# Performance work log

Measured on AMD Instinct MI355X. Metric: run time of the kernel, lower is better.

The kernel has to match this reference:

```python
import jax, jax.numpy as jnp
import numpy as np
from jax import lax


def setup_inputs() -> dict:
    key = jax.random.key(0)
    k1, k2, k3, k4 = jax.random.split(key, 4)
    B, K, Hp, Wp = 512, 64, 5, 5
    num_classes = 10
    x = jax.random.uniform(k1, (B, 1, 20, 20), dtype=jnp.float32)
    patterns = jax.random.uniform(k2, (K, 1, Hp, Wp), dtype=jnp.float32)
    w2 = jax.random.normal(k3, (1, K), dtype=jnp.float32) * 0.1
    b2 = jnp.zeros((1,), dtype=jnp.float32)
    wf = jax.random.normal(k4, (num_classes, 400), dtype=jnp.float32) * 0.05
    bf = jnp.zeros((num_classes,), dtype=jnp.float32)
    return {"x": x, "patterns": patterns, "w2": w2, "b2": b2, "wf": wf, "bf": bf}


def _geneo1(patterns, x):
    # patterns: (K,1,Hp,Wp), x: (B,1,H,W). Same-padded sliding L1 similarity.
    K, _, Hp, Wp = patterns.shape
    P = Hp * Wp
    xp = jnp.pad(x, ((0, 0), (0, 0), (Hp // 2, Hp // 2), (Wp // 2, Wp // 2)))
    # (B, P, H_out, W_out); C=1 so feature order is row-major over (Hp,Wp),
    # matching torch's unfold(2,Hp,1).unfold(3,Wp,1).reshape(-1).
    patches = lax.conv_general_dilated_patches(xp, (Hp, Wp), (1, 1), "VALID")
    pat = patterns.reshape(K, P)
    # (B,K,H_out,W_out): mean_|p| |pattern - patch|
    diff = jnp.abs(pat[None, :, :, None, None] - patches[:, None, :, :, :]).mean(axis=2)
    return 1.0 - diff


def _channel_wise_max(t):
    B, K, H, W = t.shape
    flat = t.reshape(B, K, H * W)
    idx = jnp.argmax(flat, axis=2)                      # (B,K)
    mask = jax.nn.one_hot(idx, H * W, dtype=flat.dtype) # (B,K,HW)
    return (flat * mask).reshape(B, K, H, W)


def reference(x, patterns, w2, b2, wf, bf):
    Fk = _geneo1(patterns, x)            # (B,K,20,20)
    cwm = _channel_wise_max(Fk)          # (B,K,20,20)
    # GENEO2: Linear(K,1) over channel dim (applied on (B,H,W,K))
    t = jnp.einsum("bkhw,ok->bhwo", cwm, w2) + b2   # (B,20,20,1)
    t = jax.nn.sigmoid(t)
    out = t.reshape(t.shape[0], -1) @ wf.T + bf      # (B,num_classes)
    return jax.nn.sigmoid(out)
```

## Files before the change

### kernel.cpp

```cpp
#include <hip/hip_runtime.h>
#include <math.h>

#define NB 512
#define NK 64
#define HW 400
#define NC 10

__device__ __forceinline__ unsigned sad16(unsigned a, unsigned b, unsigned c) {
#if __has_builtin(__builtin_amdgcn_sad_u16)
    return __builtin_amdgcn_sad_u16(a, b, c);
#else
    unsigned d;
    asm("v_sad_u16 %0, %1, %2, %3" : "=v"(d) : "v"(a), "v"(b), "v"(c));
    return d;
#endif
}

__global__ __launch_bounds__(1024, 1) void geneo_mlp_kernel(
    const float* __restrict__ x,
    const float* __restrict__ patterns,
    const float* __restrict__ w2,
    const float* __restrict__ b2,
    const float* __restrict__ wf,
    const float* __restrict__ bf,
    float* __restrict__ out)
{
    __shared__ __align__(16) unsigned xq4[4][576];
    __shared__ __align__(16) unsigned pqd4[4][552];
    __shared__ __align__(16) float pat_lds[NK * 25];
    __shared__ unsigned redbest[16][NK];
    __shared__ float2 pixcv[NK];
    __shared__ float colsum[NC];
    __shared__ float redout[NC];

    const int tid  = threadIdx.x;
    const int b    = blockIdx.x;
    const int lane = tid & 63;
    const int wave = tid >> 6;

    if (tid < 576) {
        const int h = tid / 24, w = tid - h * 24;
        float v = 0.f;
        if (h >= 2 && h < 22 && w >= 2 && w < 22)
            v = x[b * HW + (h - 2) * 20 + (w - 2)];
        xq4[0][tid] = (unsigned)(v * 65535.f + 0.5f);
    } else if (tid < 976) {
        const int i = tid - 576;
        reinterpret_cast<float4*>(pat_lds)[i] =
            reinterpret_cast<const float4*>(patterns)[i];
    }
    __syncthreads();

    for (int i = tid; i < 3 * 576; i += 1024) {
        const int j = i / 576 + 1;
        const int w = i - (j - 1) * 576;
        int src = w + j; if (src > 575) src = 575;
        xq4[j][w] = xq4[0][src];
    }
    __syncthreads();

    for (int i = tid; i < 4 * 552; i += 1024) {
        const int j = i / 552;
        const int w = i - j * 552;
        pqd4[j][w] = xq4[j][w] | (xq4[j][w + 24] << 16);
    }

    unsigned vp01[5], vp23[5], p4v[5];
    #pragma unroll
    for (int c = 0; c < 5; ++c) {
        const unsigned q0 = (unsigned)(pat_lds[lane * 25 +  0 + c] * 65535.f + 0.5f);
        const unsigned q1 = (unsigned)(pat_lds[lane * 25 +  5 + c] * 65535.f + 0.5f);
        const unsigned q2 = (unsigned)(pat_lds[lane * 25 + 10 + c] * 65535.f + 0.5f);
        const unsigned q3 = (unsigned)(pat_lds[lane * 25 + 15 + c] * 65535.f + 0.5f);
        const unsigned q4 = (unsigned)(pat_lds[lane * 25 + 20 + c] * 65535.f + 0.5f);
        vp01[c] = q0 | (q1 << 16);
        vp23[c] = q2 | (q3 << 16);
        p4v[c]  = q4;
    }
    __syncthreads();

    const int tr   = wave >> 2;
    const int tc   = wave & 3;
    const int base = 4 * tc;
    unsigned best  = 0xFFFFFFFFu;

    #pragma unroll 1
    for (int r = 0; r < 5; ++r) {
        const int h = tr * 5 + r;
        const unsigned* r01 = &pqd4[tc][h * 24 + base];
        const unsigned* r23 = &pqd4[tc][(h + 2) * 24 + base];
        const unsigned* r4  = &xq4[tc][(h + 4) * 24 + base];
        uint4 A0 = *reinterpret_cast<const uint4*>(r01);
        uint4 A1 = *reinterpret_cast<const uint4*>(r01 + 4);
        unsigned A8 = r01[8];
        uint4 B0 = *reinterpret_cast<const uint4*>(r23);
        uint4 B1 = *reinterpret_cast<const uint4*>(r23 + 4);
        unsigned B8 = r23[8];
        uint4 C0 = *reinterpret_cast<const uint4*>(r4);
        uint4 C1 = *reinterpret_cast<const uint4*>(r4 + 4);
        unsigned C8 = r4[8];
        const unsigned W01[9] = {A0.x, A0.y, A0.z, A0.w, A1.x, A1.y, A1.z, A1.w, A8};
        const unsigned W23[9] = {B0.x, B0.y, B0.z, B0.w, B1.x, B1.y, B1.z, B1.w, B8};
        const unsigned W4 [9] = {C0.x, C0.y, C0.z, C0.w, C1.x, C1.y, C1.z, C1.w, C8};
        #pragma unroll
        for (int px = 0; px < 5; ++px) {
            unsigned s = 0;
            #pragma unroll
            for (int dx = 0; dx < 5; ++dx) {
                s = sad16(W01[px + dx], vp01[dx], s);
                s = sad16(W23[px + dx], vp23[dx], s);
                s = sad16(W4 [px + dx], p4v [dx], s);
            }
            const unsigned pk = (s << 9) | (unsigned)(h * 20 + tc * 5 + px);
            best = min(best, pk);
        }
    }
    redbest[wave][lane] = best;
    __syncthreads();

    if (wave < NC) {
        float sc = 0.f;
        for (int p = lane; p < HW; p += 64) sc += wf[wave * HW + p];
        #pragma unroll
        for (int off = 32; off >= 1; off >>= 1) sc += __shfl_down(sc, off);
        if (lane == 0) colsum[wave] = sc;
    }
    if (wave == 15) {
        unsigned b0 = redbest[0][lane];
        #pragma unroll
        for (int w = 1; w < 16; ++w) b0 = min(b0, redbest[w][lane]);
        const float F  = 1.f - (float)(b0 >> 9) * (1.f / (25.f * 65535.f));
        const float cv = F * w2[lane];
        pixcv[lane] = make_float2(cv, __int_as_float((int)(b0 & 511u)));
    }
    __syncthreads();

    if (wave == 0) {
        const int mypix = __float_as_int(pixcv[lane].y);
        float ssum = 0.f;
        int   firstj = 64;
        #pragma unroll 8
        for (int j = 0; j < NK; ++j) {
            const float2 pc = pixcv[j];
            if (__float_as_int(pc.y) == mypix) {
                ssum += pc.x;
                if (j < firstj) firstj = j;
            }
        }
        const float b2v = b2[0];
        const float t0  = 1.f / (1.f + expf(-b2v));
        const float t   = 1.f / (1.f + expf(-(b2v + ssum)));
        const float dlt = (firstj == lane) ? (t - t0) : 0.f;
        #pragma unroll
        for (int c = 0; c < NC; ++c) {
            float v = dlt * wf[c * HW + mypix];
            #pragma unroll
            for (int off = 32; off >= 1; off >>= 1) v += __shfl_down(v, off);
            if (lane == 0) redout[c] = v;
        }
    }
    __syncthreads();

    if (tid < NC) {
        const float b2v = b2[0];
        const float t0  = 1.f / (1.f + expf(-b2v));
        const float s   = t0 * colsum[tid] + redout[tid] + bf[tid];
        out[b * NC + tid] = 1.f / (1.f + expf(-s));
    }
}

extern "C" void kernel_launch(void* const* d_in, const int* in_sizes, int n_in,
                              void* d_out, int out_size, void* d_ws, size_t ws_size,
                              hipStream_t stream) {
    const float* x        = (const float*)d_in[0];
    const float* patterns = (const float*)d_in[1];
    const float* w2       = (const float*)d_in[2];
    const float* b2       = (const float*)d_in[3];
    const float* wf       = (const float*)d_in[4];
    const float* bf       = (const float*)d_in[5];
    float* out = (float*)d_out;

    geneo_mlp_kernel<<<NB, 1024, 0, stream>>>(x, patterns, w2, b2, wf, bf, out);
}
```

Baseline: 20.81 us.

## Halve block size to 512 threads and build shifted x copies directly

```diff
diff --git a/kernel.cpp b/kernel.cpp
--- a/kernel.cpp
+++ b/kernel.cpp
@@ -5,6 +5,7 @@
 #define NK 64
 #define HW 400
 #define NC 10
+#define NWAVE 8
 
 __device__ __forceinline__ unsigned sad16(unsigned a, unsigned b, unsigned c) {
 #if __has_builtin(__builtin_amdgcn_sad_u16)
@@ -16,7 +17,7 @@
 #endif
 }
 
-__global__ __launch_bounds__(1024, 1) void geneo_mlp_kernel(
+__global__ __launch_bounds__(512, 2) void geneo_mlp_kernel(
     const float* __restrict__ x,
     const float* __restrict__ patterns,
     const float* __restrict__ w2,
@@ -28,7 +29,7 @@
     __shared__ __align__(16) unsigned xq4[4][576];
     __shared__ __align__(16) unsigned pqd4[4][552];
     __shared__ __align__(16) float pat_lds[NK * 25];
-    __shared__ unsigned redbest[16][NK];
+    __shared__ unsigned redbest[NWAVE][NK];
     __shared__ float2 pixcv[NK];
     __shared__ float colsum[NC];
     __shared__ float redout[NC];
@@ -38,33 +39,31 @@
     const int lane = tid & 63;
     const int wave = tid >> 6;
 
-    if (tid < 576) {
-        const int h = tid / 24, w = tid - h * 24;
-        float v = 0.f;
-        if (h >= 2 && h < 22 && w >= 2 && w < 22)
-            v = x[b * HW + (h - 2) * 20 + (w - 2)];
-        xq4[0][tid] = (unsigned)(v * 65535.f + 0.5f);
-    } else if (tid < 976) {
-        const int i = tid - 576;
-        reinterpret_cast<float4*>(pat_lds)[i] =
-            reinterpret_cast<const float4*>(patterns)[i];
+    for (int i = tid; i < 4 * 576; i += 512) {
+        const int j = i >> 9 >> 0;
+    }
+    {
+        for (int i = tid; i < 4 * 576; i += 512) {
+            const int j = i / 576;
+            const int w = i - j * 576;
+            const int ph = w / 24;
+            const int pc = (w - ph * 24) + j;
+            float v = 0.f;
+            if (ph >= 2 && ph < 22 && pc >= 2 && pc < 22)
+                v = x[b * HW + (ph - 2) * 20 + (pc - 2)];
+            xq4[j][w] = (unsigned)(v * 65535.f + 0.5f);
+        }
+        if (tid < 400)
+            reinterpret_cast<float4*>(pat_lds)[tid] =
+                reinterpret_cast<const float4*>(patterns)[tid];
     }
     __syncthreads();
 
-    for (int i = tid; i < 3 * 576; i += 1024) {
-        const int j = i / 576 + 1;
-        const int w = i - (j - 1) * 576;
-        int src = w + j; if (src > 575) src = 575;
-        xq4[j][w] = xq4[0][src];
-    }
-    __syncthreads();
-
-    for (int i = tid; i < 4 * 552; i += 1024) {
+    for (int i = tid; i < 4 * 552; i += 512) {
         const int j = i / 552;
         const int w = i - j * 552;
         pqd4[j][w] = xq4[j][w] | (xq4[j][w + 24] << 16);
     }
-
     unsigned vp01[5], vp23[5], p4v[5];
     #pragma unroll
     for (int c = 0; c < 5; ++c) {
@@ -85,8 +84,8 @@
     unsigned best  = 0xFFFFFFFFu;
 
     #pragma unroll 1
-    for (int r = 0; r < 5; ++r) {
-        const int h = tr * 5 + r;
+    for (int r = 0; r < 10; ++r) {
+        const int h = tr * 10 + r;
         const unsigned* r01 = &pqd4[tc][h * 24 + base];
         const unsigned* r23 = &pqd4[tc][(h + 2) * 24 + base];
         const unsigned* r4  = &xq4[tc][(h + 4) * 24 + base];
@@ -118,20 +117,19 @@
     redbest[wave][lane] = best;
     __syncthreads();
 
-    if (wave < NC) {
+    for (int c = wave; c < NC; c += NWAVE) {
         float sc = 0.f;
-        for (int p = lane; p < HW; p += 64) sc += wf[wave * HW + p];
+        for (int p = lane; p < HW; p += 64) sc += wf[c * HW + p];
         #pragma unroll
         for (int off = 32; off >= 1; off >>= 1) sc += __shfl_down(sc, off);
-        if (lane == 0) colsum[wave] = sc;
+        if (lane == 0) colsum[c] = sc;
     }
-    if (wave == 15) {
+    if (wave == NWAVE - 1) {
         unsigned b0 = redbest[0][lane];
         #pragma unroll
-        for (int w = 1; w < 16; ++w) b0 = min(b0, redbest[w][lane]);
+        for (int w = 1; w < NWAVE; ++w) b0 = min(b0, redbest[w][lane]);
         const float F  = 1.f - (float)(b0 >> 9) * (1.f / (25.f * 65535.f));
-        const float cv = F * w2[lane];
-        pixcv[lane] = make_float2(cv, __int_as_float((int)(b0 & 511u)));
+        pixcv[lane] = make_float2(F * w2[lane], __int_as_float((int)(b0 & 511u)));
     }
     __syncthreads();
 
@@ -180,5 +178,5 @@
     const float* bf       = (const float*)d_in[5];
     float* out = (float*)d_out;
 
-    geneo_mlp_kernel<<<NB, 1024, 0, stream>>>(x, patterns, w2, b2, wf, bf, out);
+    geneo_mlp_kernel<<<NB, 512, 0, stream>>>(x, patterns, w2, b2, wf, bf, out);
 }
```

New measurement: 22.09 us. 6.1% more time.
